# Optimization experiments

Measured on AMD Instinct MI355X. Metric: run time of the kernel, lower is better.

The kernel has to match this reference:

```python
import jax, jax.numpy as jnp
import numpy as np

B, S, D = 32, 2048, 768   # batch, seq_len, hidden_dim
NL, NF = 512, 64          # num_lines, num_functions


def setup_inputs() -> dict:
    key = jax.random.key(0)
    k = jax.random.split(key, 4)
    hidden_states = jax.random.normal(k[0], (B, S, D), dtype=jnp.float32)
    proj_W = jax.random.normal(k[1], (D, D), dtype=jnp.float32) * 0.02
    proj_b = jnp.zeros((D,), dtype=jnp.float32)
    # start <= end per pair, indices in-range
    line_boundaries = jnp.sort(jax.random.randint(k[2], (B, NL, 2), 0, S), axis=-1)
    function_boundaries = jnp.sort(jax.random.randint(k[3], (B, NF, 2), 0, NL), axis=-1)
    return dict(hidden_states=hidden_states, proj_W=proj_W, proj_b=proj_b,
                line_boundaries=line_boundaries, function_boundaries=function_boundaries)


def segment_mean(x, boundaries):
    """Mean of x[b, start:end] per segment; zeros when start >= end.
    x: [B, S, D]; boundaries: [B, N, 2] -> [B, N, D].
    Uses an exclusive prefix-sum so all segments are reduced in one pass."""
    csum = jnp.concatenate([jnp.zeros_like(x[:, :1]), jnp.cumsum(x, axis=1)], axis=1)  # [B, S+1, D]
    start = boundaries[..., 0]
    end = boundaries[..., 1]
    take = lambda idx: jnp.take_along_axis(csum, idx[..., None], axis=1)  # [B, N, D]
    seg_sum = take(end) - take(start)
    length = (end - start).astype(x.dtype)[..., None]
    return jnp.where(length > 0, seg_sum / jnp.maximum(length, 1.0), jnp.zeros_like(seg_sum))


def reference(hidden_states, proj_W, proj_b, line_boundaries, function_boundaries):
    # CodeEncoder projection of pretrained hidden states (no complexity features)
    token_emb = hidden_states @ proj_W + proj_b                     # [B, S, D]
    # _encode_lines: per-boundary token mean
    line_emb = segment_mean(token_emb, line_boundaries)             # [B, NL, D]
    # _encode_functions: per-boundary line mean
    func_emb = segment_mean(line_emb, function_boundaries)          # [B, NF, D]
    # AdaptiveAvgPool1d(1) over the function axis
    file_emb = jnp.mean(func_emb, axis=1)                           # [B, D]
    return token_emb, line_emb, func_emb, file_emb
```

## Files before the change

kernel.cpp:

```cpp
#include <hip/hip_runtime.h>
#include <hip/hip_bf16.h>

#define Bq 32
#define Sq 2048
#define Dq 768
#define NLq 512
#define NFq 64
#define SCHUNKS 16
#define LCHUNKS 8

typedef unsigned short u16;
typedef __attribute__((ext_vector_type(4))) unsigned short us4;
typedef __attribute__((ext_vector_type(8))) short s16x8;
typedef __attribute__((ext_vector_type(4))) float f32x4;

static __device__ __forceinline__ u16 f2bf(float f) {
  unsigned int u = __builtin_bit_cast(unsigned int, f);
  u += 0x7fffu + ((u >> 16) & 1u);
  return (u16)(u >> 16);
}

static __device__ __forceinline__ void gload16(const void* g, void* l) {
  __builtin_amdgcn_global_load_lds(
      (const __attribute__((address_space(1))) unsigned int*)g,
      (__attribute__((address_space(3))) unsigned int*)l, 16, 0, 0);
}

__global__ __launch_bounds__(256) void cvta_kernel(const float* __restrict__ hs,
                                                   u16* __restrict__ Abf) {
  const size_t i = (size_t)blockIdx.x * 256 + threadIdx.x;
  const float4 v = ((const float4*)hs)[i];
  us4 o;
  o.x = f2bf(v.x); o.y = f2bf(v.y); o.z = f2bf(v.z); o.w = f2bf(v.w);
  ((us4*)Abf)[i] = o;
}

__global__ __launch_bounds__(256) void wt_kernel(const float* __restrict__ W,
                                                 u16* __restrict__ Wt) {
  int idx = blockIdx.x * 256 + threadIdx.x;
  int n = idx / Dq, k = idx % Dq;
  Wt[idx] = f2bf(W[(size_t)k * Dq + n]);
}

__global__ __launch_bounds__(256) void gemm_kernel(const u16* __restrict__ Abf,
                                                   const u16* __restrict__ Wt,
                                                   const float* __restrict__ bias,
                                                   float* __restrict__ C,
                                                   float* __restrict__ part16) {
  __shared__ u16 As[128 * 32];
  __shared__ u16 Bs[128 * 32];
  __shared__ float ps[2][128];
  const int tid = threadIdx.x;
  const int gn0 = blockIdx.x * 128;
  const int gm0 = blockIdx.y * 128;
  const int wave = tid >> 6, lane = tid & 63;
  const int lm = lane & 15, quad = lane >> 4;
  const int wm = (wave & 1) * 64, wn = (wave >> 1) * 64;

  const char* ga0 = (const char*)Abf + (size_t)(gm0 + (tid >> 2)) * (Dq * 2) + (tid & 3) * 16;
  const char* ga1 = ga0 + (size_t)64 * (Dq * 2);
  const char* gb0 = (const char*)Wt + (size_t)(gn0 + (tid >> 2)) * (Dq * 2) + (tid & 3) * 16;
  const char* gb1 = gb0 + (size_t)64 * (Dq * 2);
  char* lA = (char*)As + wave * 1024;
  char* lB = (char*)Bs + wave * 1024;

  f32x4 acc[4][4] = {};

  for (int kk = 0; kk < Dq / 32; ++kk) {
    __syncthreads();
    gload16(ga0, lA);
    gload16(ga1, lA + 4096);
    gload16(gb0, lB);
    gload16(gb1, lB + 4096);
    ga0 += 64; ga1 += 64; gb0 += 64; gb1 += 64;
    __syncthreads();

    s16x8 af[4], bfr[4];
#pragma unroll
    for (int i = 0; i < 4; ++i)
      af[i] = *(const s16x8*)&As[(wm + i * 16 + lm) * 32 + quad * 8];
#pragma unroll
    for (int i = 0; i < 4; ++i)
      bfr[i] = *(const s16x8*)&Bs[(wn + i * 16 + lm) * 32 + quad * 8];
#pragma unroll
    for (int mi = 0; mi < 4; ++mi)
#pragma unroll
      for (int ni = 0; ni < 4; ++ni)
        acc[mi][ni] = __builtin_amdgcn_mfma_f32_16x16x32_bf16(af[mi], bfr[ni],
                                                              acc[mi][ni], 0, 0, 0);
  }

#pragma unroll
  for (int ni = 0; ni < 4; ++ni) {
    const int gn = gn0 + wn + ni * 16 + lm;
    const float bv = bias[gn];
    float psum = 0.f;
#pragma unroll
    for (int mi = 0; mi < 4; ++mi) {
#pragma unroll
      for (int r = 0; r < 4; ++r) {
        const int gm = gm0 + wm + mi * 16 + quad * 4 + r;
        const float cv = acc[mi][ni][r] + bv;
        C[(size_t)gm * Dq + gn] = cv;
        psum += cv;
      }
    }
    psum += __shfl_xor(psum, 16);
    psum += __shfl_xor(psum, 32);
    if (lane < 16) ps[wave & 1][wn + ni * 16 + lm] = psum;
  }
  __syncthreads();
  if (tid < 128) {
    const int b = gm0 >> 11;
    const int sc = (gm0 >> 7) & 15;
    part16[((size_t)b * SCHUNKS + sc) * Dq + gn0 + tid] = ps[0][tid] + ps[1][tid];
  }
}

__global__ __launch_bounds__(256) void scan_kernel(float* __restrict__ p, int C) {
  const int idx = blockIdx.x * 256 + threadIdx.x;
  const int b = idx / Dq, d = idx % Dq;
  float run = 0.f;
  for (int c = 0; c < C; ++c) {
    const size_t o = ((size_t)b * C + c) * Dq + d;
    const float v = p[o];
    p[o] = run;
    run += v;
  }
}

__global__ __launch_bounds__(256) void csum_kernel(const float* __restrict__ tok,
                                                   const float* __restrict__ part16,
                                                   float* __restrict__ csum) {
  const int sc = blockIdx.x, dc = blockIdx.y, b = blockIdx.z;
  const int d = dc * 256 + threadIdx.x;
  const float* src = tok + ((size_t)b * Sq + sc * 128) * Dq + d;
  float* dst = csum + ((size_t)b * (Sq + 1) + sc * 128 + 1) * Dq + d;
  float run = part16[((size_t)b * SCHUNKS + sc) * Dq + d];
  if (sc == 0) csum[(size_t)b * (Sq + 1) * Dq + d] = 0.f;
  for (int s0 = 0; s0 < 128; s0 += 8) {
    float v[8];
#pragma unroll
    for (int i = 0; i < 8; ++i) v[i] = src[(size_t)(s0 + i) * Dq];
#pragma unroll
    for (int i = 0; i < 8; ++i) {
      run += v[i];
      dst[(size_t)(s0 + i) * Dq] = run;
    }
  }
}

__global__ __launch_bounds__(64) void line_kernel(const float* __restrict__ csum,
                                                  const int* __restrict__ lb,
                                                  float* __restrict__ lemb,
                                                  float* __restrict__ lpart) {
  __shared__ int sb[128];
  const int lc = blockIdx.x, d64 = blockIdx.y, b = blockIdx.z;
  const int tid = threadIdx.x;
  if (tid < 32)
    ((int4*)sb)[tid] = ((const int4*)(lb + ((size_t)b * NLq + lc * 64) * 2))[tid];
  __syncthreads();
  const int d = d64 * 64 + tid;
  const float* cs = csum + (size_t)b * (Sq + 1) * Dq + d;
  float* le = lemb + ((size_t)b * NLq + lc * 64) * Dq + d;
  float sum = 0.f;
  for (int n0 = 0; n0 < 64; n0 += 8) {
    float vs[8], ve[8];
    int len[8];
#pragma unroll
    for (int i = 0; i < 8; ++i) {
      const int s0 = sb[2 * (n0 + i)], s1 = sb[2 * (n0 + i) + 1];
      len[i] = s1 - s0;
      vs[i] = cs[(size_t)s0 * Dq];
      ve[i] = cs[(size_t)s1 * Dq];
    }
#pragma unroll
    for (int i = 0; i < 8; ++i) {
      const float v = len[i] > 0 ? (ve[i] - vs[i]) / (float)len[i] : 0.f;
      le[(size_t)(n0 + i) * Dq] = v;
      sum += v;
    }
  }
  lpart[((size_t)b * LCHUNKS + lc) * Dq + d] = sum;
}

__global__ __launch_bounds__(256) void lcsum_kernel(const float* __restrict__ lemb,
                                                    const float* __restrict__ lpart,
                                                    float* __restrict__ lcsum) {
  const int lc = blockIdx.x, dc = blockIdx.y, b = blockIdx.z;
  const int d = dc * 256 + threadIdx.x;
  const float* src = lemb + ((size_t)b * NLq + lc * 64) * Dq + d;
  float* dst = lcsum + ((size_t)b * (NLq + 1) + lc * 64 + 1) * Dq + d;
  float run = lpart[((size_t)b * LCHUNKS + lc) * Dq + d];
  if (lc == 0) lcsum[(size_t)b * (NLq + 1) * Dq + d] = 0.f;
  for (int n0 = 0; n0 < 64; n0 += 8) {
    float v[8];
#pragma unroll
    for (int i = 0; i < 8; ++i) v[i] = src[(size_t)(n0 + i) * Dq];
#pragma unroll
    for (int i = 0; i < 8; ++i) {
      run += v[i];
      dst[(size_t)(n0 + i) * Dq] = run;
    }
  }
}

__global__ __launch_bounds__(64) void func_kernel(const float* __restrict__ lcsum,
                                                  const int* __restrict__ fb,
                                                  float* __restrict__ femb,
                                                  float* __restrict__ file) {
  __shared__ int sb[NFq * 2];
  const int tid = threadIdx.x;
  const int d64 = blockIdx.x, b = blockIdx.y;
  const int d = d64 * 64 + tid;
  if (tid < NFq * 2 / 4)
    ((int4*)sb)[tid] = ((const int4*)(fb + (size_t)b * NFq * 2))[tid];
  __syncthreads();
  const float* lc = lcsum + (size_t)b * (NLq + 1) * Dq + d;
  float* fe = femb + (size_t)b * NFq * Dq + d;
  float acc = 0.f;
#pragma unroll 8
  for (int f = 0; f < NFq; ++f) {
    const int l0 = sb[2 * f], l1 = sb[2 * f + 1];
    const float v = l1 > l0 ? (lc[(size_t)l1 * Dq] - lc[(size_t)l0 * Dq]) / (float)(l1 - l0)
                            : 0.f;
    fe[(size_t)f * Dq] = v;
    acc += v;
  }
  file[(size_t)b * Dq + d] = acc * (1.f / (float)NFq);
}

extern "C" void kernel_launch(void* const* d_in, const int* in_sizes, int n_in,
                              void* d_out, int out_size, void* d_ws, size_t ws_size,
                              hipStream_t stream) {
  const float* hs   = (const float*)d_in[0];
  const float* W    = (const float*)d_in[1];
  const float* bias = (const float*)d_in[2];
  const int* lb     = (const int*)d_in[3];
  const int* fb     = (const int*)d_in[4];

  float* out = (float*)d_out;
  float* token = out;
  float* line  = token + (size_t)Bq * Sq * Dq;
  float* func  = line + (size_t)Bq * NLq * Dq;
  float* file  = func + (size_t)Bq * NFq * Dq;

  char* ws = (char*)d_ws;
  float* csum   = (float*)ws;
  u16*   Abf    = (u16*)ws;
  float* lcsum  = (float*)(ws + 201498624);
  float* part16 = lcsum;
  u16*   Wt     = (u16*)(ws + 201498624 + 50442240);
  float* lpart  = (float*)Wt;

  cvta_kernel<<<(Bq * Sq * Dq / 4) / 256, 256, 0, stream>>>(hs, Abf);
  wt_kernel<<<(Dq * Dq) / 256, 256, 0, stream>>>(W, Wt);
  gemm_kernel<<<dim3(Dq / 128, (Bq * Sq) / 128), 256, 0, stream>>>(Abf, Wt, bias, token, part16);
  scan_kernel<<<(Bq * Dq) / 256, 256, 0, stream>>>(part16, SCHUNKS);
  csum_kernel<<<dim3(SCHUNKS, 3, Bq), 256, 0, stream>>>(token, part16, csum);
  line_kernel<<<dim3(LCHUNKS, 12, Bq), 64, 0, stream>>>(csum, lb, line, lpart);
  scan_kernel<<<(Bq * Dq) / 256, 256, 0, stream>>>(lpart, LCHUNKS);
  lcsum_kernel<<<dim3(LCHUNKS, 3, Bq), 256, 0, stream>>>(line, lpart, lcsum);
  func_kernel<<<dim3(12, Bq), 64, 0, stream>>>(lcsum, fb, func, file);
}
```

Measured before the change: 676.0 us.

## Fuse fp32-to-bf16 conversion into GEMM and compute chunk prefix sums in epilogue

```diff
diff --git a/kernel.cpp b/kernel.cpp
--- a/kernel.cpp
+++ b/kernel.cpp
@@ -1,5 +1,4 @@
 #include <hip/hip_runtime.h>
-#include <hip/hip_bf16.h>
 
 #define Bq 32
 #define Sq 2048
@@ -10,7 +9,9 @@
 #define LCHUNKS 8
 
 typedef unsigned short u16;
+typedef unsigned int u32;
 typedef __attribute__((ext_vector_type(4))) unsigned short us4;
+typedef __attribute__((ext_vector_type(4))) unsigned int u32x4;
 typedef __attribute__((ext_vector_type(8))) short s16x8;
 typedef __attribute__((ext_vector_type(4))) float f32x4;
 
@@ -24,15 +25,6 @@
   __builtin_amdgcn_global_load_lds(
       (const __attribute__((address_space(1))) unsigned int*)g,
       (__attribute__((address_space(3))) unsigned int*)l, 16, 0, 0);
-}
-
-__global__ __launch_bounds__(256) void cvta_kernel(const float* __restrict__ hs,
-                                                   u16* __restrict__ Abf) {
-  const size_t i = (size_t)blockIdx.x * 256 + threadIdx.x;
-  const float4 v = ((const float4*)hs)[i];
-  us4 o;
-  o.x = f2bf(v.x); o.y = f2bf(v.y); o.z = f2bf(v.z); o.w = f2bf(v.w);
-  ((us4*)Abf)[i] = o;
 }
 
 __global__ __launch_bounds__(256) void wt_kernel(const float* __restrict__ W,
@@ -42,12 +34,13 @@
   Wt[idx] = f2bf(W[(size_t)k * Dq + n]);
 }
 
-__global__ __launch_bounds__(256) void gemm_kernel(const u16* __restrict__ Abf,
-                                                   const u16* __restrict__ Wt,
-                                                   const float* __restrict__ bias,
-                                                   float* __restrict__ C,
-                                                   float* __restrict__ part16) {
-  __shared__ u16 As[128 * 32];
+__global__ __launch_bounds__(256, 3) void gemm_kernel(const float* __restrict__ A,
+                                                      const u16* __restrict__ Wt,
+                                                      const float* __restrict__ bias,
+                                                      float* __restrict__ C,
+                                                      float* __restrict__ pre,
+                                                      float* __restrict__ part16) {
+  __shared__ float Asf[128 * 32];
   __shared__ u16 Bs[128 * 32];
   __shared__ float ps[2][128];
   const int tid = threadIdx.x;
@@ -57,28 +50,44 @@
   const int lm = lane & 15, quad = lane >> 4;
   const int wm = (wave & 1) * 64, wn = (wave >> 1) * 64;
 
-  const char* ga0 = (const char*)Abf + (size_t)(gm0 + (tid >> 2)) * (Dq * 2) + (tid & 3) * 16;
-  const char* ga1 = ga0 + (size_t)64 * (Dq * 2);
+  const int arow = tid >> 3;
+  const int ah = (tid & 7) ^ (arow & 7);
+  const size_t astride = (size_t)Dq * 4;
+  const char* ga = (const char*)A + (size_t)(gm0 + arow) * astride + ah * 16;
   const char* gb0 = (const char*)Wt + (size_t)(gn0 + (tid >> 2)) * (Dq * 2) + (tid & 3) * 16;
   const char* gb1 = gb0 + (size_t)64 * (Dq * 2);
-  char* lA = (char*)As + wave * 1024;
+  char* lA = (char*)Asf + wave * 1024;
   char* lB = (char*)Bs + wave * 1024;
 
   f32x4 acc[4][4] = {};
+  const int ax = lm & 7;
 
   for (int kk = 0; kk < Dq / 32; ++kk) {
     __syncthreads();
-    gload16(ga0, lA);
-    gload16(ga1, lA + 4096);
+    gload16(ga, lA);
+    gload16(ga + 32 * astride, lA + 4096);
+    gload16(ga + 64 * astride, lA + 8192);
+    gload16(ga + 96 * astride, lA + 12288);
     gload16(gb0, lB);
     gload16(gb1, lB + 4096);
-    ga0 += 64; ga1 += 64; gb0 += 64; gb1 += 64;
+    ga += 128; gb0 += 64; gb1 += 64;
     __syncthreads();
 
     s16x8 af[4], bfr[4];
 #pragma unroll
-    for (int i = 0; i < 4; ++i)
-      af[i] = *(const s16x8*)&As[(wm + i * 16 + lm) * 32 + quad * 8];
+    for (int i = 0; i < 4; ++i) {
+      const float* rowA = Asf + (wm + i * 16 + lm) * 32;
+      f32x4 alo = *(const f32x4*)(rowA + (((2 * quad) ^ ax) << 2));
+      f32x4 ahi = *(const f32x4*)(rowA + (((2 * quad + 1) ^ ax) << 2));
+      u32 p0, p1, p2, p3;
+      asm("v_cvt_pk_bf16_f32 %0, %1, %2" : "=v"(p0) : "v"(alo.x), "v"(alo.y));
+      asm("v_cvt_pk_bf16_f32 %0, %1, %2" : "=v"(p1) : "v"(alo.z), "v"(alo.w));
+      asm("v_cvt_pk_bf16_f32 %0, %1, %2" : "=v"(p2) : "v"(ahi.x), "v"(ahi.y));
+      asm("v_cvt_pk_bf16_f32 %0, %1, %2" : "=v"(p3) : "v"(ahi.z), "v"(ahi.w));
+      u32x4 u;
+      u.x = p0; u.y = p1; u.z = p2; u.w = p3;
+      af[i] = __builtin_bit_cast(s16x8, u);
+    }
 #pragma unroll
     for (int i = 0; i < 4; ++i)
       bfr[i] = *(const s16x8*)&Bs[(wn + i * 16 + lm) * 32 + quad * 8];
@@ -114,6 +123,33 @@
     const int b = gm0 >> 11;
     const int sc = (gm0 >> 7) & 15;
     part16[((size_t)b * SCHUNKS + sc) * Dq + gn0 + tid] = ps[0][tid] + ps[1][tid];
+  }
+
+#pragma unroll
+  for (int ni = 0; ni < 4; ++ni) {
+    const int col = wn + ni * 16 + lm;
+    const float bv = bias[gn0 + col];
+    float em = wm ? ps[0][col] : 0.f;
+#pragma unroll
+    for (int mi = 0; mi < 4; ++mi) {
+      const float v0 = acc[mi][ni][0] + bv, v1 = acc[mi][ni][1] + bv,
+                  v2 = acc[mi][ni][2] + bv, v3 = acc[mi][ni][3] + bv;
+      const float qs = v0 + v1 + v2 + v3;
+      const float t1 = __shfl_up(qs, 16);
+      const float i1 = qs + (quad >= 1 ? t1 : 0.f);
+      const float t2 = __shfl_up(i1, 32);
+      const float iq = i1 + (quad >= 2 ? t2 : 0.f);
+      const float eq = iq - qs;
+      const float tot = __shfl(iq, 48 + lm);
+      const float base = em + eq;
+      em += tot;
+      const float P0 = base + v0, P1 = P0 + v1, P2 = P1 + v2, P3 = P2 + v3;
+      const size_t rowb = (size_t)(gm0 + wm + mi * 16 + quad * 4) * Dq + gn0 + col;
+      pre[rowb] = P0;
+      pre[rowb + Dq] = P1;
+      pre[rowb + 2 * (size_t)Dq] = P2;
+      pre[rowb + 3 * (size_t)Dq] = P3;
+    }
   }
 }
 
@@ -129,39 +165,23 @@
   }
 }
 
-__global__ __launch_bounds__(256) void csum_kernel(const float* __restrict__ tok,
-                                                   const float* __restrict__ part16,
-                                                   float* __restrict__ csum) {
-  const int sc = blockIdx.x, dc = blockIdx.y, b = blockIdx.z;
-  const int d = dc * 256 + threadIdx.x;
-  const float* src = tok + ((size_t)b * Sq + sc * 128) * Dq + d;
-  float* dst = csum + ((size_t)b * (Sq + 1) + sc * 128 + 1) * Dq + d;
-  float run = part16[((size_t)b * SCHUNKS + sc) * Dq + d];
-  if (sc == 0) csum[(size_t)b * (Sq + 1) * Dq + d] = 0.f;
-  for (int s0 = 0; s0 < 128; s0 += 8) {
-    float v[8];
-#pragma unroll
-    for (int i = 0; i < 8; ++i) v[i] = src[(size_t)(s0 + i) * Dq];
-#pragma unroll
-    for (int i = 0; i < 8; ++i) {
-      run += v[i];
-      dst[(size_t)(s0 + i) * Dq] = run;
-    }
-  }
-}
-
-__global__ __launch_bounds__(64) void line_kernel(const float* __restrict__ csum,
+__global__ __launch_bounds__(64) void line_kernel(const float* __restrict__ pre,
+                                                  const float* __restrict__ part,
                                                   const int* __restrict__ lb,
                                                   float* __restrict__ lemb,
                                                   float* __restrict__ lpart) {
   __shared__ int sb[128];
+  __shared__ float soff[SCHUNKS][64];
   const int lc = blockIdx.x, d64 = blockIdx.y, b = blockIdx.z;
   const int tid = threadIdx.x;
   if (tid < 32)
     ((int4*)sb)[tid] = ((const int4*)(lb + ((size_t)b * NLq + lc * 64) * 2))[tid];
+  const int d = d64 * 64 + tid;
+#pragma unroll
+  for (int sc = 0; sc < SCHUNKS; ++sc)
+    soff[sc][tid] = part[((size_t)b * SCHUNKS + sc) * Dq + d];
   __syncthreads();
-  const int d = d64 * 64 + tid;
-  const float* cs = csum + (size_t)b * (Sq + 1) * Dq + d;
+  const float* pb = pre + (size_t)b * Sq * Dq + d;
   float* le = lemb + ((size_t)b * NLq + lc * 64) * Dq + d;
   float sum = 0.f;
   for (int n0 = 0; n0 < 64; n0 += 8) {
@@ -171,8 +191,12 @@
     for (int i = 0; i < 8; ++i) {
       const int s0 = sb[2 * (n0 + i)], s1 = sb[2 * (n0 + i) + 1];
       len[i] = s1 - s0;
-      vs[i] = cs[(size_t)s0 * Dq];
-      ve[i] = cs[(size_t)s1 * Dq];
+      const int t0 = s0 > 0 ? s0 - 1 : 0;
+      const int t1 = s1 > 0 ? s1 - 1 : 0;
+      const float a0 = pb[(size_t)t0 * Dq] + soff[t0 >> 7][tid];
+      const float a1 = pb[(size_t)t1 * Dq] + soff[t1 >> 7][tid];
+      vs[i] = s0 > 0 ? a0 : 0.f;
+      ve[i] = a1;
     }
 #pragma unroll
     for (int i = 0; i < 8; ++i) {
@@ -246,19 +270,17 @@
   float* file  = func + (size_t)Bq * NFq * Dq;
 
   char* ws = (char*)d_ws;
-  float* csum   = (float*)ws;
-  u16*   Abf    = (u16*)ws;
-  float* lcsum  = (float*)(ws + 201498624);
-  float* part16 = lcsum;
-  u16*   Wt     = (u16*)(ws + 201498624 + 50442240);
-  float* lpart  = (float*)Wt;
-
-  cvta_kernel<<<(Bq * Sq * Dq / 4) / 256, 256, 0, stream>>>(hs, Abf);
+  float* precsum = (float*)ws;
+  float* lcsum   = (float*)(ws + 201498624);
+  float* part16  = lcsum;
+  u16*   Wt      = (u16*)(ws + 201498624 + 50442240);
+  float* lpart   = (float*)Wt;
+
   wt_kernel<<<(Dq * Dq) / 256, 256, 0, stream>>>(W, Wt);
-  gemm_kernel<<<dim3(Dq / 128, (Bq * Sq) / 128), 256, 0, stream>>>(Abf, Wt, bias, token, part16);
+  gemm_kernel<<<dim3(Dq / 128, (Bq * Sq) / 128), 256, 0, stream>>>(hs, Wt, bias, token,
+                                                                   precsum, part16);
   scan_kernel<<<(Bq * Dq) / 256, 256, 0, stream>>>(part16, SCHUNKS);
-  csum_kernel<<<dim3(SCHUNKS, 3, Bq), 256, 0, stream>>>(token, part16, csum);
-  line_kernel<<<dim3(LCHUNKS, 12, Bq), 64, 0, stream>>>(csum, lb, line, lpart);
+  line_kernel<<<dim3(LCHUNKS, 12, Bq), 64, 0, stream>>>(precsum, part16, lb, line, lpart);
   scan_kernel<<<(Bq * Dq) / 256, 256, 0, stream>>>(lpart, LCHUNKS);
   lcsum_kernel<<<dim3(LCHUNKS, 3, Bq), 256, 0, stream>>>(line, lpart, lcsum);
   func_kernel<<<dim3(12, Bq), 64, 0, stream>>>(lcsum, fb, func, file);
```

Result: slower. 690.6 us (+2.2%).
